# Performance work log

Hardware: AMD Instinct MI355X
Metric: run time of the kernel (lower is better)

Reference implementation:

```python
import jax, jax.numpy as jnp
import numpy as np

D_MODEL = 1024
NUM_HEADS = 16
HEAD_DIM = D_MODEL // NUM_HEADS  # 64
ROPE_THETA = 10000.0
BATCH = 2
SEQ = 2048
NEG_INF = -1e30


def setup_inputs() -> dict:
    key = jax.random.key(0)
    ks = jax.random.split(key, 6)
    std = 1.0 / np.sqrt(D_MODEL)
    x = jax.random.normal(ks[0], (BATCH, SEQ, D_MODEL), dtype=jnp.float32)
    wq = jax.random.normal(ks[1], (D_MODEL, D_MODEL), dtype=jnp.float32) * std
    wk = jax.random.normal(ks[2], (D_MODEL, D_MODEL), dtype=jnp.float32) * std
    wv = jax.random.normal(ks[3], (D_MODEL, D_MODEL), dtype=jnp.float32) * std
    wo = jax.random.normal(ks[4], (D_MODEL, D_MODEL), dtype=jnp.float32) * std
    token_positions = jnp.broadcast_to(jnp.arange(SEQ, dtype=jnp.int32)[None, :], (BATCH, SEQ))
    return {"x": x, "token_positions": token_positions, "wq": wq, "wk": wk, "wv": wv, "wo": wo}


def _apply_rope(t, token_positions):
    # t: (B, H, S, head_dim), token_positions: (B, S)
    half = HEAD_DIM // 2
    inv_freq = 1.0 / (ROPE_THETA ** (2.0 * jnp.arange(half, dtype=jnp.float32) / HEAD_DIM))
    angles = token_positions.astype(jnp.float32)[..., None] * inv_freq  # (B, S, half)
    cos = jnp.cos(angles)[:, None, :, :]  # (B, 1, S, half)
    sin = jnp.sin(angles)[:, None, :, :]
    tp = t.reshape(*t.shape[:-1], half, 2)  # interleaved pairs
    x1, x2 = tp[..., 0], tp[..., 1]
    r1 = x1 * cos - x2 * sin
    r2 = x1 * sin + x2 * cos
    return jnp.stack([r1, r2], axis=-1).reshape(t.shape)


def reference(x, token_positions, wq, wk, wv, wo):
    B, S, D = x.shape
    H, hd = NUM_HEADS, HEAD_DIM
    # projections (Linear: y = x @ W.T, no bias)
    q = (x @ wq.T).reshape(B, S, H, hd).transpose(0, 2, 1, 3)  # (B, H, S, hd)
    k = (x @ wk.T).reshape(B, S, H, hd).transpose(0, 2, 1, 3)
    v = (x @ wv.T).reshape(B, S, H, hd).transpose(0, 2, 1, 3)
    # RoPE on Q, K
    q = _apply_rope(q, token_positions)
    k = _apply_rope(k, token_positions)
    # causal scaled dot-product attention
    scores = jnp.einsum("bhqd,bhkd->bhqk", q, k) / jnp.sqrt(jnp.float32(hd))
    mask = jnp.tril(jnp.ones((S, S), dtype=bool))
    scores = jnp.where(mask, scores, NEG_INF)
    probs = jax.nn.softmax(scores, axis=-1)
    attn = jnp.einsum("bhqk,bhkd->bhqd", probs, v)  # (B, H, S, hd)
    attn = attn.transpose(0, 2, 1, 3).reshape(B, S, D)
    return attn @ wo.T
```

## Files before the change

### kernel.cpp

```cpp
#include <hip/hip_runtime.h>
#include <stdint.h>
#include <math.h>

#define SEQ 2048
#define NH 16
#define DM 1024

typedef __bf16 bf16x8 __attribute__((ext_vector_type(8)));
typedef __bf16 bf16x2 __attribute__((ext_vector_type(2)));
typedef short s16x4 __attribute__((ext_vector_type(4)));
typedef short s16x8 __attribute__((ext_vector_type(8)));
typedef float f32x4 __attribute__((ext_vector_type(4)));
typedef float f32x2 __attribute__((ext_vector_type(2)));

#define ASM_VMCNT0  asm volatile("s_waitcnt vmcnt(0)" ::: "memory")
#define ASM_LGKM0   asm volatile("s_waitcnt lgkmcnt(0)" ::: "memory")
#define ASM_BARRIER asm volatile("s_barrier" ::: "memory")

__device__ __forceinline__ unsigned short f2bf(float f) {
  union { float f; unsigned u; } v; v.f = f;
  unsigned r = v.u + 0x7fffu + ((v.u >> 16) & 1u);
  return (unsigned short)(r >> 16);
}
__device__ __forceinline__ unsigned pk2(float a, float b) {
  f32x2 v = {a, b};
  bf16x2 r = __builtin_convertvector(v, bf16x2);
  union { bf16x2 h; unsigned u; } c; c.h = r;
  return c.u;
}
__device__ __forceinline__ void load_lds16(const void* g, void* l) {
  __builtin_amdgcn_global_load_lds((__attribute__((address_space(1))) void*)g,
                                   (__attribute__((address_space(3))) void*)l,
                                   16, 0, 0);
}

__global__ void cvt_all(const float* __restrict__ x, const float* __restrict__ wq,
                        const float* __restrict__ wk, const float* __restrict__ wv,
                        const float* __restrict__ wo, unsigned short* __restrict__ ws) {
  const int i = blockIdx.x * blockDim.x + threadIdx.x;
  const int off = i * 4;
  const float* src;
  unsigned short* dst;
  if (off < 4194304) {
    src = x + off;  dst = ws + off;
  } else {
    const int r = off - 4194304;
    const int w = r >> 20, o = r & 1048575;
    const float* tabs[4] = {wq, wk, wv, wo};
    src = tabs[w] + o;  dst = ws + 4194304 + (w << 20) + o;
  }
  const float4 v = *(const float4*)src;
  uint2 u;
  u.x = pk2(v.x, v.y);
  u.y = pk2(v.z, v.w);
  *(uint2*)dst = u;
}

__launch_bounds__(256, 3)
__global__ void gemm_qkv(const unsigned short* __restrict__ X,
                         const unsigned short* __restrict__ W3,
                         unsigned short* __restrict__ Qr,
                         unsigned short* __restrict__ Kr,
                         unsigned short* __restrict__ Vt,
                         const int* __restrict__ tp) {
  __shared__ __align__(16) char smem[32768];

  const int t = threadIdx.x;
  const int lane = t & 63, wave = t >> 6;
  const int quad = lane >> 4, l16 = lane & 15;
  const int m0 = blockIdx.y * 128, n0 = blockIdx.x * 128;
  const int wm = (wave >> 1) * 64, wn = (wave & 1) * 64;

  f32x4 acc[4][4];
#pragma unroll
  for (int i = 0; i < 4; i++)
#pragma unroll
    for (int j = 0; j < 4; j++) { acc[i][j][0]=0.f; acc[i][j][1]=0.f; acc[i][j][2]=0.f; acc[i][j][3]=0.f; }

  const int rr = t >> 2;
  const int cc = (t & 3) * 8;

#define QKV_STAGE(bufidx, k0_) do {                                               \
    char* a_ = smem + (bufidx) * 8192;                                            \
    char* b_ = smem + 16384 + (bufidx) * 8192;                                    \
    _Pragma("unroll")                                                             \
    for (int i_ = 0; i_ < 2; i_++) {                                              \
      load_lds16(X  + (uint64_t)(m0 + i_ * 64 + rr) * 1024 + (k0_) + cc,          \
                 a_ + i_ * 4096 + wave * 1024);                                   \
      load_lds16(W3 + (uint64_t)(n0 + i_ * 64 + rr) * 1024 + (k0_) + cc,          \
                 b_ + i_ * 4096 + wave * 1024);                                   \
    }                                                                             \
  } while (0)

  QKV_STAGE(0, 0);

  for (int k0 = 0; k0 < 1024; k0 += 32) {
    const int buf = (k0 >> 5) & 1;
    ASM_VMCNT0;
    ASM_BARRIER;
    if (k0 + 32 < 1024) QKV_STAGE(buf ^ 1, k0 + 32);
    char* As = smem + buf * 8192;
    char* Bs = smem + 16384 + buf * 8192;

    bf16x8 af[4], bfr[4];
#pragma unroll
    for (int i = 0; i < 4; i++) {
      af[i]  = *(const bf16x8*)(As + (wm + i * 16 + l16) * 64 + quad * 16);
      bfr[i] = *(const bf16x8*)(Bs + (wn + i * 16 + l16) * 64 + quad * 16);
    }
#pragma unroll
    for (int i = 0; i < 4; i++)
#pragma unroll
      for (int j = 0; j < 4; j++)
        acc[i][j] = __builtin_amdgcn_mfma_f32_16x16x32_bf16(af[i], bfr[j], acc[i][j], 0, 0, 0);
  }
#undef QKV_STAGE

  if (n0 < 2048) {
    unsigned short* dst = (n0 < 1024) ? Qr : Kr;
    float fr[4]; int dd[4], hh[4];
#pragma unroll
    for (int j = 0; j < 4; j++) {
      const int n = n0 + wn + j * 16 + l16;
      dd[j] = n & 63;
      hh[j] = (n & 1023) >> 6;
      fr[j] = __builtin_amdgcn_exp2f(-0.20762050594f * (float)(dd[j] & ~1)) * 0.15915494309f;
    }
    const float sgnodd = (l16 & 1) ? 1.f : -1.f;
#pragma unroll
    for (int i = 0; i < 4; i++) {
#pragma unroll
      for (int r = 0; r < 4; r++) {
        const int m = m0 + wm + i * 16 + quad * 4 + r;
        const int s = m & 2047, b = m >> 11;
        const float posf = (float)tp[m];
#pragma unroll
        for (int j = 0; j < 4; j++) {
          const float v = acc[i][j][r];
          const float p = __shfl_xor(v, 1);
          float rev = posf * fr[j];
          rev -= floorf(rev);
          float sn, cs;
          asm("v_sin_f32 %0, %1" : "=v"(sn) : "v"(rev));
          asm("v_cos_f32 %0, %1" : "=v"(cs) : "v"(rev));
          const float rv = fmaf(v, cs, p * sn * sgnodd);
          dst[((uint64_t)((b * NH + hh[j]) * SEQ + s)) * 64 + dd[j]] = f2bf(rv);
        }
      }
    }
  } else {
#pragma unroll
    for (int i = 0; i < 4; i++) {
      const int m = m0 + wm + i * 16 + quad * 4;
      const int s = m & 2047, b = m >> 11;
      const int sl = s & 63;
      const int qv = (sl >> 2) & 3, nv = sl >> 4;
      const int g = (s & ~63) + qv * 16 + (nv >> 1) * 8 + (nv & 1) * 4;
#pragma unroll
      for (int j = 0; j < 4; j++) {
        const int n = n0 - 2048 + wn + j * 16 + l16;
        const int h = n >> 6, d = n & 63;
        uint2 w;
        w.x = pk2(acc[i][j][0], acc[i][j][1]);
        w.y = pk2(acc[i][j][2], acc[i][j][3]);
        *(uint2*)(Vt + ((uint64_t)((b * NH + h) * 64 + d)) * SEQ + g) = w;
      }
    }
  }
}

__launch_bounds__(512, 2)
__global__ void gemm_ao(const unsigned short* __restrict__ A,
                        const unsigned short* __restrict__ B,
                        float* __restrict__ C) {
  __shared__ __align__(16) char smem[32768];

  const int t = threadIdx.x;
  const int lane = t & 63, wave = t >> 6;
  const int quad = lane >> 4, l16 = lane & 15;
  const int id = blockIdx.y * 8 + blockIdx.x;
  const int k = id & 7;
  const int tt = id >> 3;
  const int m0 = (k * 4 + (tt & 3)) * 128;
  const int n0 = (tt >> 2) * 128;
  const int wm = (wave >> 2) * 64;
  const int wn = (wave & 3) * 32;

  f32x4 acc[4][2];
#pragma unroll
  for (int i = 0; i < 4; i++)
#pragma unroll
    for (int j = 0; j < 2; j++) { acc[i][j][0]=0.f; acc[i][j][1]=0.f; acc[i][j][2]=0.f; acc[i][j][3]=0.f; }

  const int rr = t >> 2;
  const int cc = (t & 3) * 8;

#define AO_STAGE(bufidx, k0_) do {                                               \
    char* a_ = smem + (bufidx) * 8192;                                            \
    char* b_ = smem + 16384 + (bufidx) * 8192;                                    \
    load_lds16(A + (uint64_t)(m0 + rr) * 1024 + (k0_) + cc, a_ + wave * 1024);    \
    load_lds16(B + (uint64_t)(n0 + rr) * 1024 + (k0_) + cc, b_ + wave * 1024);    \
  } while (0)

  AO_STAGE(0, 0);

  for (int k0 = 0; k0 < 1024; k0 += 32) {
    const int buf = (k0 >> 5) & 1;
    ASM_VMCNT0;
    ASM_BARRIER;
    if (k0 + 32 < 1024) AO_STAGE(buf ^ 1, k0 + 32);
    char* As = smem + buf * 8192;
    char* Bs = smem + 16384 + buf * 8192;

    bf16x8 af[4], bfr[2];
#pragma unroll
    for (int i = 0; i < 4; i++)
      af[i]  = *(const bf16x8*)(As + (wm + i * 16 + l16) * 64 + quad * 16);
#pragma unroll
    for (int j = 0; j < 2; j++)
      bfr[j] = *(const bf16x8*)(Bs + (wn + j * 16 + l16) * 64 + quad * 16);
#pragma unroll
    for (int i = 0; i < 4; i++)
#pragma unroll
      for (int j = 0; j < 2; j++)
        acc[i][j] = __builtin_amdgcn_mfma_f32_16x16x32_bf16(af[i], bfr[j], acc[i][j], 0, 0, 0);
  }
#undef AO_STAGE

#pragma unroll
  for (int i = 0; i < 4; i++)
#pragma unroll
    for (int j = 0; j < 2; j++)
#pragma unroll
      for (int r = 0; r < 4; r++) {
        const int m = m0 + wm + i * 16 + quad * 4 + r;
        const int n = n0 + wn + j * 16 + l16;
        C[(uint64_t)m * DM + n] = acc[i][j][r];
      }
}

__launch_bounds__(256, 4)
__global__ void flash_attn(const unsigned short* __restrict__ Q,
                           const unsigned short* __restrict__ K,
                           const unsigned short* __restrict__ Vt,
                           unsigned short* __restrict__ Oa) {
  __shared__ __align__(16) char smem[32768];

  const int t = threadIdx.x;
  const int lane = t & 63, wid = t >> 6;
  const int quad = lane >> 4, l16 = lane & 15;
  const int kw = wid & 1;
  const int qw = wid >> 1;
  const int u = blockIdx.x;
  const int m = u >> 5;
  const int tq = (m < 16) ? (31 - m) : (m - 16);
  const int bh = u & 31;
  const uint64_t base = (uint64_t)bh * (SEQ * 64);
  const int qb = tq * 64;
  const int ng = tq + 1;
  const int b = bh >> 4, h = bh & 15;
  const int qlo = qb + qw * 32;

  bf16x8 qf[2][2];
  {
    const unsigned short* qp0 = Q + base + (uint64_t)(qlo + l16) * 64 + quad * 8;
    qf[0][0] = *(const bf16x8*)qp0;  qf[0][1] = *(const bf16x8*)(qp0 + 32);
    const unsigned short* qp1 = Q + base + (uint64_t)(qlo + 16 + l16) * 64 + quad * 8;
    qf[1][0] = *(const bf16x8*)qp1;  qf[1][1] = *(const bf16x8*)(qp1 + 32);
  }

  f32x4 o[2][4];
#pragma unroll
  for (int qg = 0; qg < 2; qg++)
#pragma unroll
    for (int db = 0; db < 4; db++) { o[qg][db][0]=0.f; o[qg][db][1]=0.f; o[qg][db][2]=0.f; o[qg][db][3]=0.f; }
  float lI0 = 0.f, lI1 = 0.f;

  const int sr8 = lane >> 3;
  const int sc = ((lane & 7) ^ sr8) * 8;
  const int swz = (l16 & 7);

#define STAGE(bufidx, kb_) do {                                                   \
    _Pragma("unroll")                                                             \
    for (int i_ = 0; i_ < 2; i_++) {                                              \
      const int r_ = wid * 16 + i_ * 8 + sr8;                                     \
      load_lds16(K  + base + (uint64_t)((kb_) + r_) * 64 + sc,                    \
                 smem + (bufidx) * 8192 + wid * 2048 + i_ * 1024);                \
      load_lds16(Vt + base + (uint64_t)r_ * SEQ + (kb_) + sc,                     \
                 smem + 16384 + (bufidx) * 8192 + wid * 2048 + i_ * 1024);        \
    }                                                                             \
  } while (0)

  STAGE(0, 0);

  const float c1 = 0.18033688011f;

  for (int it = 0; it < ng; it++) {
    const int kb = it * 64;
    const int buf = it & 1;
    ASM_VMCNT0;
    ASM_BARRIER;
    if (it + 1 < ng) STAGE(buf ^ 1, (it + 1) * 64);
    char* ks = smem + buf * 8192;
    char* vs = smem + 16384 + buf * 8192;

    int nv = ((qlo + 31 - kb) >> 4) + 1 - 2 * kw;
    nv = nv > 2 ? 2 : (nv < 0 ? 0 : nv);
    const bool diag = (kb + kw * 32 + 31) > qlo;

    if (nv > 0) {
      f32x4 sf0[2], sf1[2];
      float ls0 = 0.f, ls1 = 0.f;
#pragma unroll
      for (int nbp = 0; nbp < 2; nbp++) {
        if (nbp < nv) {
          f32x4 s0; s0[0]=0.f; s0[1]=0.f; s0[2]=0.f; s0[3]=0.f;
          f32x4 s1; s1[0]=0.f; s1[1]=0.f; s1[2]=0.f; s1[3]=0.f;
#pragma unroll
          for (int kk = 0; kk < 2; kk++) {
            bf16x8 kfr = *(const bf16x8*)(ks + ((2 * kw + nbp) * 16 + l16) * 128 +
                                          (((kk * 4 + quad) ^ swz) * 16));
            s0 = __builtin_amdgcn_mfma_f32_16x16x32_bf16(kfr, qf[0][kk], s0, 0, 0, 0);
            s1 = __builtin_amdgcn_mfma_f32_16x16x32_bf16(kfr, qf[1][kk], s1, 0, 0, 0);
          }
          if (diag) {
#pragma unroll
            for (int r = 0; r < 4; r++) {
              const int key = kb + (2 * kw + nbp) * 16 + quad * 4 + r;
              const float p0 = (key <= qlo + l16)      ? __builtin_amdgcn_exp2f(s0[r] * c1) : 0.f;
              const float p1 = (key <= qlo + 16 + l16) ? __builtin_amdgcn_exp2f(s1[r] * c1) : 0.f;
              sf0[nbp][r] = p0;  ls0 += p0;
              sf1[nbp][r] = p1;  ls1 += p1;
            }
          } else {
#pragma unroll
            for (int r = 0; r < 4; r++) {
              const float p0 = __builtin_amdgcn_exp2f(s0[r] * c1);
              const float p1 = __builtin_amdgcn_exp2f(s1[r] * c1);
              sf0[nbp][r] = p0;  ls0 += p0;
              sf1[nbp][r] = p1;  ls1 += p1;
            }
          }
        }
      }
      lI0 += ls0;  lI1 += ls1;

      union { uint2 u; s16x4 h; } a0, b0, a1, b1;
      a0.u.x = pk2(sf0[0][0], sf0[0][1]);  a0.u.y = pk2(sf0[0][2], sf0[0][3]);
      b0.u.x = pk2(sf1[0][0], sf1[0][1]);  b0.u.y = pk2(sf1[0][2], sf1[0][3]);
      const bool hi = (nv > 1);
      if (hi) {
        a1.u.x = pk2(sf0[1][0], sf0[1][1]);  a1.u.y = pk2(sf0[1][2], sf0[1][3]);
        b1.u.x = pk2(sf1[1][0], sf1[1][1]);  b1.u.y = pk2(sf1[1][2], sf1[1][3]);
      }
#pragma unroll
      for (int db = 0; db < 4; db++) {
        s16x8 vv = *(const s16x8*)(vs + (db * 16 + l16) * 128 +
                                   (((quad * 2 + kw) ^ swz) * 16));
        s16x4 vlo = __builtin_shufflevector(vv, vv, 0, 1, 2, 3);
        o[0][db] = __builtin_amdgcn_mfma_f32_16x16x16bf16_1k(vlo, a0.h, o[0][db], 0, 0, 0);
        o[1][db] = __builtin_amdgcn_mfma_f32_16x16x16bf16_1k(vlo, b0.h, o[1][db], 0, 0, 0);
        if (hi) {
          s16x4 vhi = __builtin_shufflevector(vv, vv, 4, 5, 6, 7);
          o[0][db] = __builtin_amdgcn_mfma_f32_16x16x16bf16_1k(vhi, a1.h, o[0][db], 0, 0, 0);
          o[1][db] = __builtin_amdgcn_mfma_f32_16x16x16bf16_1k(vhi, b1.h, o[1][db], 0, 0, 0);
        }
      }
    }
  }
#undef STAGE

  float lr0 = lI0;  lr0 += __shfl_xor(lr0, 16);  lr0 += __shfl_xor(lr0, 32);
  float lr1 = lI1;  lr1 += __shfl_xor(lr1, 16);  lr1 += __shfl_xor(lr1, 32);

  ASM_LGKM0;
  ASM_BARRIER;
  if (kw) {
    char* pbase = smem + qw * 8192;
#pragma unroll
    for (int qg = 0; qg < 2; qg++)
#pragma unroll
      for (int db = 0; db < 4; db++)
        *(f32x4*)(pbase + (qg * 4 + db) * 1024 + quad * 256 + l16 * 16) = o[qg][db];
    if (quad == 0) {
      *(float*)(smem + 16384 + qw * 128 + l16 * 4) = lr0;
      *(float*)(smem + 16384 + qw * 128 + 64 + l16 * 4) = lr1;
    }
  }
  ASM_LGKM0;
  ASM_BARRIER;
  if (!kw) {
    char* pbase = smem + qw * 8192;
#pragma unroll
    for (int qg = 0; qg < 2; qg++) {
      const float lpart = *(const float*)(smem + 16384 + qw * 128 + qg * 64 + l16 * 4);
      const float invl = 1.0f / ((qg ? lr1 : lr0) + lpart);
      const int qrow = qlo + qg * 16 + l16;
      unsigned short* orow = Oa + ((uint64_t)(b * SEQ + qrow)) * DM + h * 64 + quad * 4;
#pragma unroll
      for (int db = 0; db < 4; db++) {
        const f32x4 p = *(const f32x4*)(pbase + (qg * 4 + db) * 1024 + quad * 256 + l16 * 16);
        uint2 w;
        w.x = pk2((o[qg][db][0] + p[0]) * invl, (o[qg][db][1] + p[1]) * invl);
        w.y = pk2((o[qg][db][2] + p[2]) * invl, (o[qg][db][3] + p[3]) * invl);
        *(uint2*)(orow + db * 16) = w;
      }
    }
  }
}

extern "C" void kernel_launch(void* const* d_in, const int* in_sizes, int n_in,
                              void* d_out, int out_size, void* d_ws, size_t ws_size,
                              hipStream_t stream) {
  const float* x  = (const float*)d_in[0];
  const int* tp   = (const int*)d_in[1];
  const float* wq = (const float*)d_in[2];
  const float* wk = (const float*)d_in[3];
  const float* wv = (const float*)d_in[4];
  const float* wo = (const float*)d_in[5];
  float* out = (float*)d_out;

  unsigned short* ws = (unsigned short*)d_ws;
  unsigned short* xb  = ws;
  unsigned short* w3b = ws + 4194304;
  unsigned short* wob = ws + 7340032;
  unsigned short* Qr  = ws + 8388608;
  unsigned short* Kr  = ws + 12582912;
  unsigned short* Vt  = ws + 16777216;
  unsigned short* At  = ws + 20971520;

  cvt_all<<<8192, 256, 0, stream>>>(x, wq, wk, wv, wo, ws);
  gemm_qkv<<<dim3(24, 32), 256, 0, stream>>>(xb, w3b, Qr, Kr, Vt, tp);
  flash_attn<<<1024, 256, 0, stream>>>(Qr, Kr, Vt, At);
  gemm_ao<<<dim3(8, 32), 512, 0, stream>>>(At, wob, out);
}
```

Measured before the change: 165.7 us.

## Read K and V fragments directly from global memory instead of LDS staging

Drops the double-buffered LDS staging of K and Vt tiles in the flash attention loop, along with its per-iteration waitcnt and barrier. Each wave now loads its MFMA fragments straight from global memory and relies on L1/L2 for reuse across waves. The Vt layout permutation in the projection epilogue is changed so that direct contiguous 16-byte reads yield the right operand order. LDS use shrinks to the epilogue reduction buffer, but global load latency is no longer hidden by prefetch.

```diff
diff --git a/kernel.cpp b/kernel.cpp
--- a/kernel.cpp
+++ b/kernel.cpp
@@ -155,7 +155,7 @@
       const int s = m & 2047, b = m >> 11;
       const int sl = s & 63;
       const int qv = (sl >> 2) & 3, nv = sl >> 4;
-      const int g = (s & ~63) + qv * 16 + (nv >> 1) * 8 + (nv & 1) * 4;
+      const int g = (s & ~63) + (nv >> 1) * 32 + qv * 8 + (nv & 1) * 4;
 #pragma unroll
       for (int j = 0; j < 4; j++) {
         const int n = n0 - 2048 + wn + j * 16 + l16;
@@ -244,7 +244,7 @@
                            const unsigned short* __restrict__ K,
                            const unsigned short* __restrict__ Vt,
                            unsigned short* __restrict__ Oa) {
-  __shared__ __align__(16) char smem[32768];
+  __shared__ __align__(16) char smem[16640];
 
   const int t = threadIdx.x;
   const int lane = t & 63, wid = t >> 6;
@@ -276,33 +276,10 @@
     for (int db = 0; db < 4; db++) { o[qg][db][0]=0.f; o[qg][db][1]=0.f; o[qg][db][2]=0.f; o[qg][db][3]=0.f; }
   float lI0 = 0.f, lI1 = 0.f;
 
-  const int sr8 = lane >> 3;
-  const int sc = ((lane & 7) ^ sr8) * 8;
-  const int swz = (l16 & 7);
-
-#define STAGE(bufidx, kb_) do {                                                   \
-    _Pragma("unroll")                                                             \
-    for (int i_ = 0; i_ < 2; i_++) {                                              \
-      const int r_ = wid * 16 + i_ * 8 + sr8;                                     \
-      load_lds16(K  + base + (uint64_t)((kb_) + r_) * 64 + sc,                    \
-                 smem + (bufidx) * 8192 + wid * 2048 + i_ * 1024);                \
-      load_lds16(Vt + base + (uint64_t)r_ * SEQ + (kb_) + sc,                     \
-                 smem + 16384 + (bufidx) * 8192 + wid * 2048 + i_ * 1024);        \
-    }                                                                             \
-  } while (0)
-
-  STAGE(0, 0);
-
   const float c1 = 0.18033688011f;
 
   for (int it = 0; it < ng; it++) {
     const int kb = it * 64;
-    const int buf = it & 1;
-    ASM_VMCNT0;
-    ASM_BARRIER;
-    if (it + 1 < ng) STAGE(buf ^ 1, (it + 1) * 64);
-    char* ks = smem + buf * 8192;
-    char* vs = smem + 16384 + buf * 8192;
 
     int nv = ((qlo + 31 - kb) >> 4) + 1 - 2 * kw;
     nv = nv > 2 ? 2 : (nv < 0 ? 0 : nv);
@@ -318,8 +295,8 @@
           f32x4 s1; s1[0]=0.f; s1[1]=0.f; s1[2]=0.f; s1[3]=0.f;
 #pragma unroll
           for (int kk = 0; kk < 2; kk++) {
-            bf16x8 kfr = *(const bf16x8*)(ks + ((2 * kw + nbp) * 16 + l16) * 128 +
-                                          (((kk * 4 + quad) ^ swz) * 16));
+            bf16x8 kfr = *(const bf16x8*)(K + base +
+                (uint64_t)(kb + (2 * kw + nbp) * 16 + l16) * 64 + kk * 32 + quad * 8);
             s0 = __builtin_amdgcn_mfma_f32_16x16x32_bf16(kfr, qf[0][kk], s0, 0, 0, 0);
             s1 = __builtin_amdgcn_mfma_f32_16x16x32_bf16(kfr, qf[1][kk], s1, 0, 0, 0);
           }
@@ -355,8 +332,8 @@
       }
 #pragma unroll
       for (int db = 0; db < 4; db++) {
-        s16x8 vv = *(const s16x8*)(vs + (db * 16 + l16) * 128 +
-                                   (((quad * 2 + kw) ^ swz) * 16));
+        s16x8 vv = *(const s16x8*)(Vt + base +
+            (uint64_t)(db * 16 + l16) * SEQ + kb + kw * 32 + quad * 8);
         s16x4 vlo = __builtin_shufflevector(vv, vv, 0, 1, 2, 3);
         o[0][db] = __builtin_amdgcn_mfma_f32_16x16x16bf16_1k(vlo, a0.h, o[0][db], 0, 0, 0);
         o[1][db] = __builtin_amdgcn_mfma_f32_16x16x16bf16_1k(vlo, b0.h, o[1][db], 0, 0, 0);
@@ -368,12 +345,10 @@
       }
     }
   }
-#undef STAGE
 
   float lr0 = lI0;  lr0 += __shfl_xor(lr0, 16);  lr0 += __shfl_xor(lr0, 32);
   float lr1 = lI1;  lr1 += __shfl_xor(lr1, 16);  lr1 += __shfl_xor(lr1, 32);
 
-  ASM_LGKM0;
   ASM_BARRIER;
   if (kw) {
     char* pbase = smem + qw * 8192;
```

Result: slower. 203.6 us (+22.9%).
